# Performance work log

Hardware: AMD Instinct MI355X
Metric: run time of the kernel (lower is better)

Reference implementation:

```python
import jax, jax.numpy as jnp
import numpy as np
from jax import lax

B, T, FEAT = 8, 512, 128
D_MODEL, D_STATE, D_INNER, DT_RANK = 128, 16, 256, 8
N_LAYERS, NUM_CLASSES = 10, 35
FLAT = 64 * (FEAT // 4)  # 2048


def setup_inputs():
    keys = iter(jax.random.split(jax.random.key(0), 48))
    def nrm(shape, s=0.05):
        return jax.random.normal(next(keys), shape, jnp.float32) * s
    inp = {}
    inp['x'] = jax.random.normal(next(keys), (B, T, FEAT), jnp.float32)
    inp['lengths'] = jax.random.randint(next(keys), (B,), 0, T)
    inp['conv_w1'] = nrm((32, 1, 3, 3)); inp['conv_b1'] = nrm((32,))
    inp['bn1_s'] = 1.0 + nrm((32,)); inp['bn1_b'] = nrm((32,))
    inp['conv_w2'] = nrm((32, 32, 3, 3)); inp['conv_b2'] = nrm((32,))
    inp['bn2_s'] = 1.0 + nrm((32,)); inp['bn2_b'] = nrm((32,))
    inp['conv_w3'] = nrm((64, 32, 3, 3)); inp['conv_b3'] = nrm((64,))
    inp['bn3_s'] = 1.0 + nrm((64,)); inp['bn3_b'] = nrm((64,))
    inp['conv_w4'] = nrm((64, 64, 3, 3)); inp['conv_b4'] = nrm((64,))
    inp['bn4_s'] = 1.0 + nrm((64,)); inp['bn4_b'] = nrm((64,))
    inp['proj_w'] = nrm((D_MODEL, FLAT), 0.02); inp['proj_b'] = nrm((D_MODEL,))
    inp['proj_ln_s'] = jnp.ones((D_MODEL,)); inp['proj_ln_b'] = jnp.zeros((D_MODEL,))
    L = N_LAYERS
    inp['blk_ln_s'] = jnp.ones((L, D_MODEL)); inp['blk_ln_b'] = jnp.zeros((L, D_MODEL))
    inp['in_w'] = nrm((L, 2 * D_INNER, D_MODEL))
    inp['cw'] = nrm((L, D_INNER, 4)); inp['cb'] = nrm((L, D_INNER))
    inp['xp_w'] = nrm((L, DT_RANK + 2 * D_STATE, D_INNER))
    inp['dt_w'] = nrm((L, D_INNER, DT_RANK))
    inp['dt_b'] = nrm((L, D_INNER)) - 4.0  # softplus(-4) ~ 0.018: realistic small dt
    inp['A_log'] = jnp.tile(jnp.log(jnp.arange(1, D_STATE + 1, dtype=jnp.float32))[None, None, :], (L, D_INNER, 1))
    inp['Dp'] = jnp.ones((L, D_INNER))
    inp['out_w'] = nrm((L, D_MODEL, D_INNER))
    inp['pre_ln_s'] = jnp.ones((D_MODEL,)); inp['pre_ln_b'] = jnp.zeros((D_MODEL,))
    inp['cls_w1'] = nrm((D_MODEL // 2, D_MODEL)); inp['cls_b1'] = nrm((D_MODEL // 2,))
    inp['cls_w2'] = nrm((NUM_CLASSES, D_MODEL // 2)); inp['cls_b2'] = nrm((NUM_CLASSES,))
    return inp


def _ln(x, s, b):
    m = jnp.mean(x, -1, keepdims=True)
    v = jnp.mean((x - m) ** 2, -1, keepdims=True)
    return (x - m) * lax.rsqrt(v + 1e-5) * s + b


def _conv2d(x, w, b):
    y = lax.conv_general_dilated(x, w, (1, 1), 'SAME', dimension_numbers=('NCHW', 'OIHW', 'NCHW'))
    return y + b[None, :, None, None]


def _bn(x, s, b):  # eval-mode BatchNorm folded to per-channel affine
    return x * s[None, :, None, None] + b[None, :, None, None]


def _pool(x, kh, kw):
    return lax.reduce_window(x, -jnp.inf, lax.max, (1, 1, kh, kw), (1, 1, kh, kw), 'VALID')


def _mamba(x, in_w, cw, cb, xp_w, dt_w, dt_b, A_log, Dp, out_w):
    bb = x.shape[0]
    xz = jnp.einsum('btd,ed->bte', x, in_w)                  # [B,T,2*d_inner]
    xm, z = jnp.split(xz, 2, axis=-1)
    # causal depthwise conv1d (torch pads both sides by 3 then truncates to T == left-pad 3)
    xc = lax.conv_general_dilated(xm.transpose(0, 2, 1), cw[:, None, :], (1,), [(3, 0)],
                                  dimension_numbers=('NCH', 'OIH', 'NCH'), feature_group_count=D_INNER)
    xc = jax.nn.silu(xc + cb[None, :, None]).transpose(0, 2, 1)  # [B,T,d_inner]
    dbc = jnp.einsum('btd,ed->bte', xc, xp_w)
    dt, Bm, Cm = jnp.split(dbc, [DT_RANK, DT_RANK + D_STATE], axis=-1)
    dt = jax.nn.softplus(jnp.einsum('btr,dr->btd', dt, dt_w) + dt_b)  # [B,T,d_inner]
    A = -jnp.exp(A_log)                                      # [d_inner,d_state]
    dA = jnp.exp(dt[..., None] * A)                          # [B,T,d,n]
    dBu = (dt * xc)[..., None] * Bm[:, :, None, :]           # [B,T,d,n]
    def step(h, inp):
        dA_t, dBu_t, C_t = inp
        h = dA_t * h + dBu_t
        return h, jnp.einsum('bdn,bn->bd', h, C_t)
    h0 = jnp.zeros((bb, D_INNER, D_STATE), x.dtype)
    _, ys = lax.scan(step, h0, (dA.transpose(1, 0, 2, 3), dBu.transpose(1, 0, 2, 3), Cm.transpose(1, 0, 2)))
    y = ys.transpose(1, 0, 2) + Dp * xc
    y = y * jax.nn.silu(z)
    return jnp.einsum('btd,ed->bte', y, out_w)


def _forward(x, lengths, conv_w1, conv_b1, bn1_s, bn1_b, conv_w2, conv_b2, bn2_s, bn2_b,
             conv_w3, conv_b3, bn3_s, bn3_b, conv_w4, conv_b4, bn4_s, bn4_b,
             proj_w, proj_b, proj_ln_s, proj_ln_b, blk_ln_s, blk_ln_b,
             in_w, cw, cb, xp_w, dt_w, dt_b, A_log, Dp, out_w,
             pre_ln_s, pre_ln_b, cls_w1, cls_b1, cls_w2, cls_b2):
    h = x.transpose(0, 2, 1)[:, None]                        # [B,1,F,T]
    h = jax.nn.silu(_bn(_conv2d(h, conv_w1, conv_b1), bn1_s, bn1_b))
    h = jax.nn.silu(_bn(_conv2d(h, conv_w2, conv_b2), bn2_s, bn2_b))
    h = _pool(h, 2, 2)
    h = jax.nn.silu(_bn(_conv2d(h, conv_w3, conv_b3), bn3_s, bn3_b))
    h = jax.nn.silu(_bn(_conv2d(h, conv_w4, conv_b4), bn4_s, bn4_b))
    h = _pool(h, 2, 1)                                       # [B,64,F/4,T/2]
    h = h.transpose(0, 3, 1, 2).reshape(h.shape[0], h.shape[3], -1)  # [B,T',64*F/4]
    h = jax.nn.silu(_ln(jnp.einsum('btf,df->btd', h, proj_w) + proj_b, proj_ln_s, proj_ln_b))
    for i in range(N_LAYERS):
        h = h + _mamba(_ln(h, blk_ln_s[i], blk_ln_b[i]), in_w[i], cw[i], cb[i], xp_w[i],
                       dt_w[i], dt_b[i], A_log[i], Dp[i], out_w[i])
    h = _ln(h, pre_ln_s, pre_ln_b)
    t_lens = jnp.clip(lengths // 2, 1)
    mask = (jnp.arange(h.shape[1])[None, :] < t_lens[:, None]).astype(h.dtype)[..., None]
    pooled = (h * mask).sum(1) / jnp.clip(mask.sum(1), 1.0)
    c = jax.nn.silu(jnp.einsum('bd,hd->bh', pooled, cls_w1) + cls_b1)
    return jnp.einsum('bh,ch->bc', c, cls_w2) + cls_b2


def reference(x, lengths, conv_w1, conv_b1, bn1_s, bn1_b, conv_w2, conv_b2, bn2_s, bn2_b,
              conv_w3, conv_b3, bn3_s, bn3_b, conv_w4, conv_b4, bn4_s, bn4_b,
              proj_w, proj_b, proj_ln_s, proj_ln_b, blk_ln_s, blk_ln_b,
              in_w, cw, cb, xp_w, dt_w, dt_b, A_log, Dp, out_w,
              pre_ln_s, pre_ln_b, cls_w1, cls_b1, cls_w2, cls_b2):
    return _forward(x, lengths, conv_w1, conv_b1, bn1_s, bn1_b, conv_w2, conv_b2, bn2_s, bn2_b,
                    conv_w3, conv_b3, bn3_s, bn3_b, conv_w4, conv_b4, bn4_s, bn4_b,
                    proj_w, proj_b, proj_ln_s, proj_ln_b, blk_ln_s, blk_ln_b,
                    in_w, cw, cb, xp_w, dt_w, dt_b, A_log, Dp, out_w,
                    pre_ln_s, pre_ln_b, cls_w1, cls_b1, cls_w2, cls_b2)
```

## Files before the change

### kernel.cpp

```cpp
#include <hip/hip_runtime.h>
#include <math.h>

#define B_ 8
#define T_ 512
#define FEAT_ 128
#define TP 256
#define DM 128
#define DI 256
#define DS 16
#define DTR 8
#define NL 10

typedef _Float16 h2 __attribute__((ext_vector_type(2)));
typedef unsigned int uint32;

__device__ __forceinline__ float fsilu(float x){ return x / (1.f + __expf(-x)); }
__device__ __forceinline__ float fsoftplus(float x){ return (x > 20.f) ? x : log1pf(__expf(x)); }

__device__ __forceinline__ uint32 pack_h2(float a, float b){
  union { h2 h; uint32 u; } cv;
  cv.h[0] = (_Float16)a; cv.h[1] = (_Float16)b;
  return cv.u;
}
__device__ __forceinline__ h2 as_h2(uint32 u){
  union { uint32 u; h2 h; } cv; cv.u = u; return cv.h;
}

template<int CTRL>
__device__ __forceinline__ float dpp_ror(float x){
  int v = __builtin_amdgcn_update_dpp(0, __float_as_int(x), CTRL, 0xF, 0xF, false);
  return __int_as_float(v);
}
__device__ __forceinline__ float rsum16(float x){
  x += dpp_ror<0x121>(x);
  x += dpp_ror<0x122>(x);
  x += dpp_ror<0x124>(x);
  x += dpp_ror<0x128>(x);
  return x;
}

__global__ void k_transpose_x(const float* __restrict__ x, float* __restrict__ xT){
  int idx = blockIdx.x*256 + threadIdx.x;
  if(idx >= B_*FEAT_*T_) return;
  int t = idx % T_; int f = (idx/T_) % FEAT_; int b = idx/(T_*FEAT_);
  xT[idx] = x[((size_t)b*T_ + t)*FEAT_ + f];
}

__device__ __forceinline__ void wt_one(const float* __restrict__ w, float* __restrict__ o,
                                       int idx, int CO, int CIN){
  int k = idx % 9; int ci = (idx/9) % CIN; int co = idx/(9*CIN);
  o[((size_t)(ci*(CO>>3) + (co>>3)))*72 + (co&7)*9 + k] = w[idx];
}
__device__ __forceinline__ void wt_pack(const float* __restrict__ w, uint32* __restrict__ o,
                                        int idx, int CO, int CIN){
  int CIN2 = CIN >> 1;
  int k = idx % 9; int ci2 = (idx/9) % CIN2; int co = idx/(9*CIN2);
  float f0 = w[((size_t)co*CIN + 2*ci2 + 0)*9 + k];
  float f1 = w[((size_t)co*CIN + 2*ci2 + 1)*9 + k];
  o[((size_t)(ci2*(CO>>3) + (co>>3)))*72 + (co&7)*9 + k] = pack_h2(f0, f1);
}
__global__ void k_wt_all(const float* __restrict__ w1, const float* __restrict__ w2,
                         const float* __restrict__ w3, const float* __restrict__ w4,
                         float* __restrict__ o1, uint32* __restrict__ o2,
                         uint32* __restrict__ o3, uint32* __restrict__ o4){
  int idx = blockIdx.x*256 + threadIdx.x;
  if(idx < 288){ wt_one(w1, o1, idx, 32, 1); return; }
  idx -= 288;
  if(idx < 4608){ wt_pack(w2, o2, idx, 32, 32); return; }
  idx -= 4608;
  if(idx < 9216){ wt_pack(w3, o3, idx, 64, 32); return; }
  idx -= 9216;
  if(idx < 18432){ wt_pack(w4, o4, idx, 64, 64); return; }
}

template<int CIN, int CO, int CPW, int CIG, int COG>
__global__ __launch_bounds__(256) void k_conv_t4(const float* __restrict__ in,
     const float* __restrict__ wt, const float* __restrict__ cb,
     const float* __restrict__ bs, const float* __restrict__ bb,
     float* __restrict__ out, int H, int W){
  constexpr int NS = CO/CPW;
  __shared__ __align__(16) float tile[CIG*360];
  int tid = threadIdx.x;
  int lane = tid & 63;
  int wav = __builtin_amdgcn_readfirstlane(tid >> 6);
  int wpr = W >> 4, hpr = H >> 4;
  int idx = blockIdx.x;
  int cog = idx % COG; idx /= COG;
  int tj = idx % wpr; idx /= wpr;
  int ti = idx % hpr; int b = idx / hpr;
  int i0 = ti*16, j0 = tj*16;
  int r = lane & 15, cg = lane >> 4;
  int wslot = cog*4 + wav;
  const float* wbase = wt + (size_t)wslot*72;
  float acc[CPW][4] = {};
  for(int cig = 0; cig < CIN; cig += CIG){
    __syncthreads();
    for(int u = tid; u < CIG*324; u += 256){
      int ci = u / 324; int rem = u - ci*324; int rr = rem / 18; int cc = rem - rr*18;
      int gi = i0 - 1 + rr, gj = j0 - 1 + cc;
      float v = 0.f;
      if(gi >= 0 && gi < H && gj >= 0 && gj < W)
        v = in[((size_t)(b*CIN + cig + ci)*H + gi)*W + gj];
      tile[ci*360 + rr*20 + cc] = v;
    }
    __syncthreads();
    for(int ci = 0; ci < CIG; ci++){
      const float4* wp4 = (const float4*)(wbase + (size_t)(cig+ci)*(NS*72));
      float4 w4q[18];
      #pragma unroll
      for(int q=0;q<18;q++) w4q[q] = wp4[q];
      const float* wf = (const float*)w4q;
      #pragma unroll
      for(int kh=0;kh<3;kh++){
        float4 a = *(const float4*)&tile[ci*360 + (r+kh)*20 + cg*4];
        float4 bv = *(const float4*)&tile[ci*360 + (r+kh)*20 + cg*4 + 4];
        float v[6] = {a.x,a.y,a.z,a.w,bv.x,bv.y};
        #pragma unroll
        for(int co=0;co<CPW;co++){
          #pragma unroll
          for(int kw=0;kw<3;kw++){
            float wv = wf[co*9 + kh*3 + kw];
            #pragma unroll
            for(int u2=0;u2<4;u2++)
              acc[co][u2] = fmaf(wv, v[kw+u2], acc[co][u2]);
          }
        }
      }
    }
  }
  int i = i0 + r;
  #pragma unroll
  for(int co=0; co<CPW; co++){
    int c = cog*(4*CPW) + wav*CPW + co;
    float s = bs[c], bias = cb[c]*s + bb[c];
    float4 o;
    o.x = fsilu(acc[co][0]*s + bias);
    o.y = fsilu(acc[co][1]*s + bias);
    o.z = fsilu(acc[co][2]*s + bias);
    o.w = fsilu(acc[co][3]*s + bias);
    *(float4*)&out[((size_t)(b*CO + c)*H + i)*W + j0 + cg*4] = o;
  }
}

template<int CIN2, int CO, int CPW, int CIG2, int COG>
__global__ __launch_bounds__(256) void k_conv_t7(const float* __restrict__ in,
     const uint32* __restrict__ wt, const float* __restrict__ cb,
     const float* __restrict__ bs, const float* __restrict__ bb,
     float* __restrict__ out, int H, int W){
  constexpr int NS = CO/CPW;
  __shared__ __align__(16) uint32 tile[CIG2*360];
  int tid = threadIdx.x;
  int lane = tid & 63;
  int wav = __builtin_amdgcn_readfirstlane(tid >> 6);
  int wpr = W >> 4, hpr = H >> 4;
  int idx = blockIdx.x;
  int cog = idx % COG; idx /= COG;
  int tj = idx % wpr; idx /= wpr;
  int ti = idx % hpr; int b = idx / hpr;
  int i0 = ti*16, j0 = tj*16;
  int r = lane & 15, cg = lane >> 4;
  int wslot = cog*4 + wav;
  const uint32* wbase = wt + (size_t)wslot*72;
  float acc[CPW][4] = {};
  for(int c2g = 0; c2g < CIN2; c2g += CIG2){
    __syncthreads();
    for(int u = tid; u < CIG2*324; u += 256){
      int ci2 = u / 324; int rem = u - ci2*324; int rr = rem / 18; int cc = rem - rr*18;
      int gi = i0 - 1 + rr, gj = j0 - 1 + cc;
      float v0 = 0.f, v1 = 0.f;
      if(gi >= 0 && gi < H && gj >= 0 && gj < W){
        const float* p = in + ((size_t)(b*(CIN2*2) + (c2g+ci2)*2)*H + gi)*W + gj;
        v0 = p[0];
        v1 = p[(size_t)H*W];
      }
      tile[ci2*360 + rr*20 + cc] = pack_h2(v0, v1);
    }
    __syncthreads();
    for(int ci2 = 0; ci2 < CIG2; ci2++){
      const uint4* wp4 = (const uint4*)(wbase + (size_t)(c2g+ci2)*(NS*72));
      uint4 w4q[18];
      #pragma unroll
      for(int q=0;q<18;q++) w4q[q] = wp4[q];
      const uint32* wf = (const uint32*)w4q;
      h2 v[3][6];
      #pragma unroll
      for(int kh=0;kh<3;kh++){
        const uint32* trow = &tile[ci2*360 + (r+kh)*20 + cg*4];
        uint4 a4 = *(const uint4*)trow;
        v[kh][0]=as_h2(a4.x); v[kh][1]=as_h2(a4.y);
        v[kh][2]=as_h2(a4.z); v[kh][3]=as_h2(a4.w);
        v[kh][4]=as_h2(trow[4]); v[kh][5]=as_h2(trow[5]);
      }
      #pragma unroll
      for(int co=0;co<CPW;co++){
        #pragma unroll
        for(int kh=0;kh<3;kh++){
          #pragma unroll
          for(int kw=0;kw<3;kw++){
            h2 wv = as_h2(wf[co*9 + kh*3 + kw]);
            #pragma unroll
            for(int u2=0;u2<4;u2++)
              acc[co][u2] = __builtin_amdgcn_fdot2(wv, v[kh][kw+u2], acc[co][u2], false);
          }
        }
      }
    }
  }
  int i = i0 + r;
  #pragma unroll
  for(int co=0; co<CPW; co++){
    int c = cog*(4*CPW) + wav*CPW + co;
    float s = bs[c], bias = cb[c]*s + bb[c];
    float4 o;
    o.x = fsilu(acc[co][0]*s + bias);
    o.y = fsilu(acc[co][1]*s + bias);
    o.z = fsilu(acc[co][2]*s + bias);
    o.w = fsilu(acc[co][3]*s + bias);
    *(float4*)&out[((size_t)(b*CO + c)*H + i)*W + j0 + cg*4] = o;
  }
}

__global__ void k_pool2x2(const float* __restrict__ in, float* __restrict__ out,
                          int C, int Hi, int Wi){
  int Ho = Hi>>1, Wo = Wi>>1;
  int total = B_*C*Ho*Wo;
  int idx = blockIdx.x*256 + threadIdx.x;
  if(idx >= total) return;
  int j = idx % Wo; int i = (idx/Wo)%Ho; int c = (idx/(Wo*Ho))%C; int b = idx/(Wo*Ho*C);
  const float* p = in + (((size_t)(b*C+c)*Hi + 2*i)*Wi + 2*j);
  out[idx] = fmaxf(fmaxf(p[0], p[1]), fmaxf(p[Wi], p[Wi+1]));
}

__global__ __launch_bounds__(256) void k_proj(const float* __restrict__ R0,
    const float* __restrict__ W, float* __restrict__ pbuf){
  __shared__ __align__(16) float As[16][33];
  __shared__ __align__(16) float Ws[16][68];
  int tid = threadIdx.x;
  int n0 = blockIdx.x*64, m0 = blockIdx.y*32;
  int kc = blockIdx.z;
  int b = m0 >> 8;
  int t_base = m0 & 255;
  int tx = tid&15, ty = tid>>4;
  float acc[2][4] = {};
  for(int k0=0; k0<256; k0+=16){
    int kg0 = kc*256 + k0;
    if(tid < 128){
      int row = tid>>2, cq = (tid&3)*4;
      #pragma unroll
      for(int c2=0;c2<4;c2++){
        int k = kg0 + cq + c2;
        int c = k>>5, hh = k&31;
        const float* p = R0 + (((size_t)(b*64+c)*64 + 2*hh)*256 + t_base + row);
        As[cq+c2][row] = fmaxf(p[0], p[256]);
      }
    } else {
      int u = tid - 128; int n = u>>1, cq = (u&1)*8;
      const float* wp = W + (size_t)(n0+n)*2048 + kg0 + cq;
      float4 v0 = *(const float4*)wp, v1 = *(const float4*)(wp+4);
      Ws[cq+0][n]=v0.x; Ws[cq+1][n]=v0.y; Ws[cq+2][n]=v0.z; Ws[cq+3][n]=v0.w;
      Ws[cq+4][n]=v1.x; Ws[cq+5][n]=v1.y; Ws[cq+6][n]=v1.z; Ws[cq+7][n]=v1.w;
    }
    __syncthreads();
    #pragma unroll
    for(int kk=0;kk<16;kk++){
      float a0 = As[kk][ty*2+0];
      float a1 = As[kk][ty*2+1];
      float4 w4 = *(const float4*)&Ws[kk][tx*4];
      float wv4[4] = {w4.x,w4.y,w4.z,w4.w};
      #pragma unroll
      for(int j=0;j<4;j++){
        acc[0][j] = fmaf(a0, wv4[j], acc[0][j]);
        acc[1][j] = fmaf(a1, wv4[j], acc[1][j]);
      }
    }
    __syncthreads();
  }
  float* pb = pbuf + (size_t)kc*2048*DM;
  #pragma unroll
  for(int iu=0;iu<2;iu++){
    int m = m0 + ty*2 + iu;
    #pragma unroll
    for(int j=0;j<4;j++){
      int n = n0 + tx*4 + j;
      pb[(size_t)m*DM + n] = acc[iu][j];
    }
  }
}

__global__ void k_lnp(const float* __restrict__ pbuf, const float* __restrict__ bias,
                      const float* __restrict__ g, const float* __restrict__ b,
                      float* __restrict__ out){
  int row = blockIdx.x;
  int t = threadIdx.x;
  float v0 = bias[t], v1 = bias[t+64];
  #pragma unroll
  for(int kc=0;kc<8;kc++){
    const float* p = pbuf + ((size_t)kc*2048 + row)*DM;
    v0 += p[t]; v1 += p[t+64];
  }
  float s = v0 + v1;
  #pragma unroll
  for(int m=32;m>=1;m>>=1) s += __shfl_xor(s, m);
  float mean = s * (1.f/128.f);
  float e0 = v0-mean, e1 = v1-mean;
  float q = e0*e0 + e1*e1;
  #pragma unroll
  for(int m=32;m>=1;m>>=1) q += __shfl_xor(q, m);
  float inv = rsqrtf(q*(1.f/128.f) + 1e-5f);
  float o0 = fsilu(e0*inv*g[t] + b[t]);
  float o1 = fsilu(e1*inv*g[t+64] + b[t+64]);
  float* po = out + (size_t)row*DM;
  po[t] = o0; po[t+64] = o1;
}

template<int SILU>
__global__ void k_ln(const float* __restrict__ in, const float* __restrict__ g,
                     const float* __restrict__ b, float* __restrict__ out){
  int row = blockIdx.x;
  int t = threadIdx.x;
  const float* p = in + (size_t)row*DM;
  float v0 = p[t], v1 = p[t+64];
  float s = v0 + v1;
  #pragma unroll
  for(int m=32;m>=1;m>>=1) s += __shfl_xor(s, m);
  float mean = s * (1.f/128.f);
  float e0 = v0-mean, e1 = v1-mean;
  float q = e0*e0 + e1*e1;
  #pragma unroll
  for(int m=32;m>=1;m>>=1) q += __shfl_xor(q, m);
  float inv = rsqrtf(q*(1.f/128.f) + 1e-5f);
  float o0 = e0*inv*g[t] + b[t];
  float o1 = e1*inv*g[t+64] + b[t+64];
  if(SILU){ o0 = fsilu(o0); o1 = fsilu(o1); }
  float* po = out + (size_t)row*DM;
  po[t] = o0; po[t+64] = o1;
}

__global__ __launch_bounds__(256) void k_lnxz(const float* __restrict__ hbuf,
    const float* __restrict__ g, const float* __restrict__ bb,
    const float* __restrict__ W, float* __restrict__ out){
  __shared__ __align__(16) float lns[32][132];
  __shared__ __align__(16) float Ws[16][68];
  int tid = threadIdx.x;
  int n0 = blockIdx.x*64, m0 = blockIdx.y*32;
  for(int u=tid; u<1024; u+=256){
    int row = u>>5, c4 = (u&31)*4;
    float4 v = *(const float4*)(hbuf + (size_t)(m0+row)*DM + c4);
    lns[row][c4] = v.x; lns[row][c4+1] = v.y; lns[row][c4+2] = v.z; lns[row][c4+3] = v.w;
  }
  __syncthreads();
  {
    int lane = tid & 63, wv = tid >> 6;
    for(int rr = wv; rr < 32; rr += 4){
      float v0 = lns[rr][lane], v1 = lns[rr][lane+64];
      float s = v0+v1;
      #pragma unroll
      for(int mm=32;mm>=1;mm>>=1) s += __shfl_xor(s,mm);
      float mean = s*(1.f/128.f);
      float e0 = v0-mean, e1 = v1-mean;
      float q = e0*e0+e1*e1;
      #pragma unroll
      for(int mm=32;mm>=1;mm>>=1) q += __shfl_xor(q,mm);
      float inv = rsqrtf(q*(1.f/128.f)+1e-5f);
      lns[rr][lane]    = e0*inv*g[lane] + bb[lane];
      lns[rr][lane+64] = e1*inv*g[lane+64] + bb[lane+64];
    }
  }
  __syncthreads();
  int tx = tid&15, ty = tid>>4;
  float acc[2][4] = {};
  for(int k0=0;k0<128;k0+=16){
    {
      int n = tid>>2, c4 = (tid&3)*4;
      float4 v = *(const float4*)(W + (size_t)(n0+n)*DM + k0 + c4);
      Ws[c4+0][n]=v.x; Ws[c4+1][n]=v.y; Ws[c4+2][n]=v.z; Ws[c4+3][n]=v.w;
    }
    __syncthreads();
    #pragma unroll
    for(int kk=0;kk<16;kk++){
      float a0 = lns[ty*2+0][k0+kk];
      float a1 = lns[ty*2+1][k0+kk];
      float4 w4 = *(const float4*)&Ws[kk][tx*4];
      float wv4[4] = {w4.x,w4.y,w4.z,w4.w};
      #pragma unroll
      for(int j=0;j<4;j++){
        acc[0][j] = fmaf(a0, wv4[j], acc[0][j]);
        acc[1][j] = fmaf(a1, wv4[j], acc[1][j]);
      }
    }
    __syncthreads();
  }
  #pragma unroll
  for(int iu=0;iu<2;iu++){
    int m = m0 + ty*2 + iu;
    float* po = out + (size_t)m*512 + n0 + tx*4;
    #pragma unroll
    for(int j=0;j<4;j++) po[j] = acc[iu][j];
  }
}

__global__ __launch_bounds__(256) void k_xproj8(const float* __restrict__ xz,
    const float* __restrict__ cw, const float* __restrict__ cb,
    const float* __restrict__ xpw, const float* __restrict__ dtw,
    const float* __restrict__ dtb_, float* __restrict__ xc_g,
    float* __restrict__ dbc_g, float* __restrict__ dt_g){
  __shared__ float xzs[11][64];
  __shared__ float As[64][9];
  __shared__ float Wp[64][41];
  __shared__ float dtin[8][9];
  __shared__ float dtw_s[256][9];
  int tid = threadIdx.x;
  int row0 = blockIdx.x*8; int b = row0 >> 8; int t0 = row0 & 255;
  int rA = tid & 7, cgA = tid >> 3;
  int dlC = tid & 63, rqC = tid >> 6;
  float acc0 = 0.f, acc1 = 0.f;
  for(int ch=0; ch<4; ch++){
    int d0 = ch*64;
    __syncthreads();
    for(int u=tid; u<11*64; u+=256){
      int rr = u>>6, dl = u&63;
      int t = t0 + rr - 3;
      xzs[rr][dl] = (t >= 0) ? xz[((size_t)(b*TP)+t)*512 + d0 + dl] : 0.f;
    }
    for(int u=tid; u<40*64; u+=256){
      int nn = u>>6, dk = u&63;
      Wp[dk][nn] = xpw[(size_t)nn*DI + d0 + dk];
    }
    __syncthreads();
    {
      float cw0 = cw[(d0+dlC)*4+0], cw1 = cw[(d0+dlC)*4+1];
      float cw2 = cw[(d0+dlC)*4+2], cw3 = cw[(d0+dlC)*4+3];
      float cbv = cb[d0+dlC];
      #pragma unroll
      for(int i=0;i<2;i++){
        int rr = rqC*2 + i;
        float a = cbv;
        a = fmaf(cw0, xzs[rr+0][dlC], a);
        a = fmaf(cw1, xzs[rr+1][dlC], a);
        a = fmaf(cw2, xzs[rr+2][dlC], a);
        a = fmaf(cw3, xzs[rr+3][dlC], a);
        float v = fsilu(a);
        As[dlC][rr] = v;
        xc_g[((size_t)row0 + rr)*DI + d0 + dlC] = v;
      }
    }
    __syncthreads();
    for(int dk=0; dk<64; dk++){
      float a = As[dk][rA];
      acc0 = fmaf(a, Wp[dk][cgA], acc0);
      if(cgA < 8) acc1 = fmaf(a, Wp[dk][cgA+32], acc1);
    }
  }
  if(cgA < 8){
    dtin[rA][cgA] = acc0;
    dbc_g[((size_t)row0 + rA)*40 + cgA + 32] = acc1;
  } else {
    dbc_g[((size_t)row0 + rA)*40 + cgA] = acc0;
  }
  for(int u=tid; u<256*8; u+=256) dtw_s[u>>3][u&7] = dtw[u];
  __syncthreads();
  {
    int d = tid;
    float bias = dtb_[d];
    float w8[8];
    #pragma unroll
    for(int k=0;k<8;k++) w8[k] = dtw_s[d][k];
    #pragma unroll
    for(int r2=0;r2<8;r2++){
      float a = bias;
      #pragma unroll
      for(int k=0;k<8;k++) a = fmaf(dtin[r2][k], w8[k], a);
      dt_g[((size_t)row0 + r2)*DI + d] = fsoftplus(a);
    }
  }
}

__global__ __launch_bounds__(1024) void k_scan4(const float* __restrict__ dtb,
      const float* __restrict__ xc, const float* __restrict__ xz,
      const float* __restrict__ dbc, const float* __restrict__ A_log,
      const float* __restrict__ Dp, float* __restrict__ y){
  __shared__ float dt_s[TP][8], xc_s[TP][8];
  __shared__ float Bs[TP][16], Cs[TP][16];
  __shared__ float Eb[8][128], Pb[8][128];
  int tid = threadIdx.x;
  int c = tid >> 7, gl = (tid >> 4) & 7, n = tid & 15;
  int dblk = blockIdx.x & 31, b = blockIdx.x >> 5;
  int d0 = dblk*8;
  size_t rbase = (size_t)b*TP;
  for(int u=tid; u<TP*8; u+=1024){
    int tt = u>>3, gg = u&7;
    size_t r = rbase + tt;
    dt_s[tt][gg] = dtb[r*DI + d0 + gg];
    xc_s[tt][gg] = xc [r*DI + d0 + gg];
  }
  for(int u=tid; u<TP*16; u+=1024){
    int tt = u>>4, nn = u&15;
    size_t r = rbase + tt;
    Bs[tt][nn] = dbc[r*40 + 8  + nn];
    Cs[tt][nn] = dbc[r*40 + 24 + nn];
  }
  __syncthreads();
  int d = d0 + gl;
  float An = -__expf(A_log[d*DS + n]);
  float h = 0.f, dtsum = 0.f;
  int tA = c*32;
  float hc[32], ev[32];
  #pragma unroll
  for(int i=0;i<32;i++){
    int t = tA + i;
    float dtv = dt_s[t][gl];
    dtsum += dtv;
    float e = __expf(dtv*An);
    ev[i] = e;
    h = fmaf(e, h, dtv*xc_s[t][gl]*Bs[t][n]);
    hc[i] = h*Cs[t][n];
  }
  Eb[c][gl*16+n] = h;
  Pb[c][gl*16+n] = __expf(An*dtsum);
  __syncthreads();
  float g = 0.f;
  for(int cp=0; cp<c; cp++)
    g = fmaf(Pb[cp][gl*16+n], g, Eb[cp][gl*16+n]);
  float Dpd = Dp[d];
  #pragma unroll
  for(int i=0;i<32;i++){
    int t = tA + i;
    g *= ev[i];
    float p = rsum16(hc[i] + g*Cs[t][n]);
    if(n==0){
      float zv = xz[(rbase+t)*512 + DI + d];
      float xcv = xc_s[t][gl];
      y[(rbase+t)*DI + d] = (p + Dpd*xcv) * fsilu(zv);
    }
  }
}

__global__ __launch_bounds__(256) void k_out16(const float* __restrict__ A,
    const float* __restrict__ W, float* __restrict__ C){
  __shared__ float As[16][17];
  __shared__ __align__(16) float Ws[16][68];
  int tid = threadIdx.x;
  int n0 = blockIdx.x*64, m0 = blockIdx.y*16;
  int tx = tid&15, ty = tid>>4;
  float acc[4] = {};
  for(int k0=0;k0<256;k0+=16){
    {
      int row = tid>>4, kk = tid&15;
      As[kk][row] = A[(size_t)(m0+row)*DI + k0 + kk];
    }
    {
      int n = tid>>2, cq = (tid&3)*4;
      float4 v = *(const float4*)(W + (size_t)(n0+n)*DI + k0 + cq);
      Ws[cq+0][n]=v.x; Ws[cq+1][n]=v.y; Ws[cq+2][n]=v.z; Ws[cq+3][n]=v.w;
    }
    __syncthreads();
    #pragma unroll
    for(int kk=0;kk<16;kk++){
      float a0 = As[kk][ty];
      float4 w4 = *(const float4*)&Ws[kk][tx*4];
      acc[0] = fmaf(a0, w4.x, acc[0]);
      acc[1] = fmaf(a0, w4.y, acc[1]);
      acc[2] = fmaf(a0, w4.z, acc[2]);
      acc[3] = fmaf(a0, w4.w, acc[3]);
    }
    __syncthreads();
  }
  int m = m0 + ty;
  float* cp = &C[(size_t)m*DM + n0 + tx*4];
  cp[0] += acc[0]; cp[1] += acc[1]; cp[2] += acc[2]; cp[3] += acc[3];
}

__global__ void k_head(const float* __restrict__ hln, const int* __restrict__ lengths,
                       const float* __restrict__ w1, const float* __restrict__ b1,
                       const float* __restrict__ w2, const float* __restrict__ b2,
                       float* __restrict__ out){
  __shared__ float pooled[DM];
  __shared__ float cbuf[64];
  int b = blockIdx.x, tid = threadIdx.x;
  int tl = lengths[b] >> 1; if(tl < 1) tl = 1;
  float s = 0.f;
  const float* p = hln + (size_t)b*TP*DM + tid;
  for(int t=0;t<tl;t++) s += p[(size_t)t*DM];
  pooled[tid] = s / (float)tl;
  __syncthreads();
  if(tid < 64){
    float a = b1[tid];
    const float* wp = w1 + tid*DM;
    for(int k=0;k<DM;k++) a = fmaf(pooled[k], wp[k], a);
    cbuf[tid] = fsilu(a);
  }
  __syncthreads();
  if(tid < 35){
    float a = b2[tid];
    const float* wp = w2 + tid*64;
    for(int k=0;k<64;k++) a = fmaf(cbuf[k], wp[k], a);
    out[b*35+tid] = a;
  }
}

extern "C" void kernel_launch(void* const* d_in, const int* in_sizes, int n_in,
                              void* d_out, int out_size, void* d_ws, size_t ws_size,
                              hipStream_t stream){
  (void)in_sizes; (void)n_in; (void)out_size; (void)ws_size;
  const float* x        = (const float*)d_in[0];
  const int*   lengths  = (const int*)  d_in[1];
  const float* conv_w1  = (const float*)d_in[2];  const float* conv_b1 = (const float*)d_in[3];
  const float* bn1_s    = (const float*)d_in[4];  const float* bn1_b   = (const float*)d_in[5];
  const float* conv_w2  = (const float*)d_in[6];  const float* conv_b2 = (const float*)d_in[7];
  const float* bn2_s    = (const float*)d_in[8];  const float* bn2_b   = (const float*)d_in[9];
  const float* conv_w3  = (const float*)d_in[10]; const float* conv_b3 = (const float*)d_in[11];
  const float* bn3_s    = (const float*)d_in[12]; const float* bn3_b   = (const float*)d_in[13];
  const float* conv_w4  = (const float*)d_in[14]; const float* conv_b4 = (const float*)d_in[15];
  const float* bn4_s    = (const float*)d_in[16]; const float* bn4_b   = (const float*)d_in[17];
  const float* proj_w   = (const float*)d_in[18]; const float* proj_b  = (const float*)d_in[19];
  const float* proj_ln_s= (const float*)d_in[20]; const float* proj_ln_b=(const float*)d_in[21];
  const float* blk_ln_s = (const float*)d_in[22]; const float* blk_ln_b =(const float*)d_in[23];
  const float* in_w     = (const float*)d_in[24];
  const float* cw       = (const float*)d_in[25]; const float* cbv     = (const float*)d_in[26];
  const float* xp_w     = (const float*)d_in[27];
  const float* dt_w     = (const float*)d_in[28]; const float* dt_b    = (const float*)d_in[29];
  const float* A_log    = (const float*)d_in[30]; const float* Dp      = (const float*)d_in[31];
  const float* out_w    = (const float*)d_in[32];
  const float* pre_ln_s = (const float*)d_in[33]; const float* pre_ln_b= (const float*)d_in[34];
  const float* cls_w1   = (const float*)d_in[35]; const float* cls_b1  = (const float*)d_in[36];
  const float* cls_w2   = (const float*)d_in[37]; const float* cls_b2  = (const float*)d_in[38];

  float* ws   = (float*)d_ws;
  float* R0   = ws;
  float* R1   = R0 + 16777216;
  float* xT   = R1 + 16777216;
  float* hbuf = xT + 524288;
  float* lnb  = hbuf + 262144;
  float* xzb  = lnb + 262144;
  float* xcb  = xzb + 1048576;
  float* dbcb = xcb + 524288;
  float* dtbb = dbcb + 81920;
  float* yb   = dtbb + 524288;
  float* wt1  = yb + 524288;
  uint32* wt2h = (uint32*)(wt1 + 288);
  uint32* wt3h = wt2h + 4608;
  uint32* wt4h = wt3h + 9216;

  k_wt_all<<<128, 256, 0, stream>>>(conv_w1, conv_w2, conv_w3, conv_w4,
                                    wt1, wt2h, wt3h, wt4h);

  k_transpose_x<<<2048, 256, 0, stream>>>(x, xT);
  k_conv_t4<1,32,8,1,1><<<8*8*32, 256, 0, stream>>>(xT, wt1, conv_b1, bn1_s, bn1_b, R0, 128, 512);
  k_conv_t7<16,32,8,4,1><<<8*8*32, 256, 0, stream>>>(R0, wt2h, conv_b2, bn2_s, bn2_b, R1, 128, 512);
  k_pool2x2<<<(8*32*64*256)/256, 256, 0, stream>>>(R1, R0, 32, 128, 512);
  k_conv_t7<16,64,8,4,2><<<8*4*16*2, 256, 0, stream>>>(R0, wt3h, conv_b3, bn3_s, bn3_b, R1, 64, 256);
  k_conv_t7<32,64,8,4,2><<<8*4*16*2, 256, 0, stream>>>(R1, wt4h, conv_b4, bn4_s, bn4_b, R0, 64, 256);

  {
    dim3 gd(2, 64, 8);
    k_proj<<<gd, 256, 0, stream>>>(R0, proj_w, R1);
  }
  k_lnp<<<2048, 64, 0, stream>>>(R1, proj_b, proj_ln_s, proj_ln_b, hbuf);

  for(int i=0;i<NL;i++){
    { dim3 gd(8, 64);
      k_lnxz<<<gd, 256, 0, stream>>>(hbuf, blk_ln_s + i*DM, blk_ln_b + i*DM,
                                     in_w + (size_t)i*512*DM, xzb); }
    k_xproj8<<<256, 256, 0, stream>>>(xzb, cw + (size_t)i*DI*4, cbv + i*DI,
                                      xp_w + (size_t)i*40*DI, dt_w + (size_t)i*DI*DTR,
                                      dt_b + i*DI, xcb, dbcb, dtbb);
    k_scan4<<<256, 1024, 0, stream>>>(dtbb, xcb, xzb, dbcb, A_log + (size_t)i*DI*DS, Dp + i*DI, yb);
    { dim3 gd(2, 128);
      k_out16<<<gd, 256, 0, stream>>>(yb, out_w + (size_t)i*DM*DI, hbuf); }
  }

  k_ln<0><<<2048, 64, 0, stream>>>(hbuf, pre_ln_s, pre_ln_b, lnb);
  k_head<<<8, 128, 0, stream>>>(lnb, lengths, cls_w1, cls_b1, cls_w2, cls_b2, (float*)d_out);
}
```

Baseline: 1.154 ms.

## Prefetch conv input slabs into registers, fuse final LayerNorm into head, widen CIG2

The t7 conv kernel now loads the next input-channel slab into registers while computing on the current shared-memory slab, a software pipeline intended to hide global load latency. The channel-group size per slab doubles from 4 to 8, so there are fewer barriers at the cost of more shared memory and registers. The separate final LayerNorm kernel is folded into the head kernel, which normalizes and pools only the valid timesteps, removing one launch and a full pass over the activations. The conv3 weight packing is rewritten oddly (wrong CO in k_wt_all, then corrected by an extra k_wt3 launch), which adds one small kernel launch.

```diff
diff --git a/kernel.cpp b/kernel.cpp
--- a/kernel.cpp
+++ b/kernel.cpp
@@ -68,9 +68,13 @@
   idx -= 288;
   if(idx < 4608){ wt_pack(w2, o2, idx, 32, 32); return; }
   idx -= 4608;
-  if(idx < 9216){ wt_pack(w3, o3, idx, 64, 32); return; }
+  if(idx < 9216){ wt_pack(w3, o3, idx, 32, 32); return; }
   idx -= 9216;
   if(idx < 18432){ wt_pack(w4, o4, idx, 64, 64); return; }
+}
+__global__ void k_wt3(const float* __restrict__ w3, uint32* __restrict__ o3){
+  int idx = blockIdx.x*256 + threadIdx.x;
+  if(idx < 9216) wt_pack(w3, o3, idx, 64, 32);
 }
 
 template<int CIN, int CO, int CPW, int CIG, int COG>
@@ -148,6 +152,9 @@
      const float* __restrict__ bs, const float* __restrict__ bb,
      float* __restrict__ out, int H, int W){
   constexpr int NS = CO/CPW;
+  constexpr int NSLAB = CIN2/CIG2;
+  constexpr int NEL = CIG2*324;
+  constexpr int NLD = (NEL + 255)/256;
   __shared__ __align__(16) uint32 tile[CIG2*360];
   int tid = threadIdx.x;
   int lane = tid & 63;
@@ -162,22 +169,46 @@
   int wslot = cog*4 + wav;
   const uint32* wbase = wt + (size_t)wslot*72;
   float acc[CPW][4] = {};
-  for(int c2g = 0; c2g < CIN2; c2g += CIG2){
-    __syncthreads();
-    for(int u = tid; u < CIG2*324; u += 256){
-      int ci2 = u / 324; int rem = u - ci2*324; int rr = rem / 18; int cc = rem - rr*18;
-      int gi = i0 - 1 + rr, gj = j0 - 1 + cc;
+  float r0[NLD], r1[NLD];
+
+  auto LOAD = [&](int c2g){
+    #pragma unroll
+    for(int l=0;l<NLD;l++){
+      int u = tid + l*256;
       float v0 = 0.f, v1 = 0.f;
-      if(gi >= 0 && gi < H && gj >= 0 && gj < W){
-        const float* p = in + ((size_t)(b*(CIN2*2) + (c2g+ci2)*2)*H + gi)*W + gj;
-        v0 = p[0];
-        v1 = p[(size_t)H*W];
-      }
-      tile[ci2*360 + rr*20 + cc] = pack_h2(v0, v1);
-    }
-    __syncthreads();
-    for(int ci2 = 0; ci2 < CIG2; ci2++){
-      const uint4* wp4 = (const uint4*)(wbase + (size_t)(c2g+ci2)*(NS*72));
+      if(u < NEL){
+        int ci2 = u/324; int rem = u - ci2*324; int rr = rem/18; int cc = rem - rr*18;
+        int gi = i0 - 1 + rr, gj = j0 - 1 + cc;
+        if(gi >= 0 && gi < H && gj >= 0 && gj < W){
+          const float* p = in + ((size_t)(b*(CIN2*2) + (c2g+ci2)*2)*H + gi)*W + gj;
+          v0 = p[0];
+          v1 = p[(size_t)H*W];
+        }
+      }
+      r0[l] = v0; r1[l] = v1;
+    }
+  };
+  auto WRITE = [&](){
+    #pragma unroll
+    for(int l=0;l<NLD;l++){
+      int u = tid + l*256;
+      if(u < NEL){
+        int ci2 = u/324; int rem = u - ci2*324; int rr = rem/18; int cc = rem - rr*18;
+        tile[ci2*360 + rr*20 + cc] = pack_h2(r0[l], r1[l]);
+      }
+    }
+  };
+
+  LOAD(0);
+  for(int s=0; s<NSLAB; s++){
+    __syncthreads();
+    WRITE();
+    __syncthreads();
+    if(s+1 < NSLAB) LOAD((s+1)*CIG2);
+    #pragma unroll
+    for(int ci2=0; ci2<CIG2; ci2++){
+      int sci2 = s*CIG2 + ci2;
+      const uint4* wp4 = (const uint4*)(wbase + (size_t)sci2*(NS*72));
       uint4 w4q[18];
       #pragma unroll
       for(int q=0;q<18;q++) w4q[q] = wp4[q];
@@ -309,29 +340,6 @@
   float inv = rsqrtf(q*(1.f/128.f) + 1e-5f);
   float o0 = fsilu(e0*inv*g[t] + b[t]);
   float o1 = fsilu(e1*inv*g[t+64] + b[t+64]);
-  float* po = out + (size_t)row*DM;
-  po[t] = o0; po[t+64] = o1;
-}
-
-template<int SILU>
-__global__ void k_ln(const float* __restrict__ in, const float* __restrict__ g,
-                     const float* __restrict__ b, float* __restrict__ out){
-  int row = blockIdx.x;
-  int t = threadIdx.x;
-  const float* p = in + (size_t)row*DM;
-  float v0 = p[t], v1 = p[t+64];
-  float s = v0 + v1;
-  #pragma unroll
-  for(int m=32;m>=1;m>>=1) s += __shfl_xor(s, m);
-  float mean = s * (1.f/128.f);
-  float e0 = v0-mean, e1 = v1-mean;
-  float q = e0*e0 + e1*e1;
-  #pragma unroll
-  for(int m=32;m>=1;m>>=1) q += __shfl_xor(q, m);
-  float inv = rsqrtf(q*(1.f/128.f) + 1e-5f);
-  float o0 = e0*inv*g[t] + b[t];
-  float o1 = e1*inv*g[t+64] + b[t+64];
-  if(SILU){ o0 = fsilu(o0); o1 = fsilu(o1); }
   float* po = out + (size_t)row*DM;
   po[t] = o0; po[t+64] = o1;
 }
@@ -570,18 +578,37 @@
   cp[0] += acc[0]; cp[1] += acc[1]; cp[2] += acc[2]; cp[3] += acc[3];
 }
 
-__global__ void k_head(const float* __restrict__ hln, const int* __restrict__ lengths,
-                       const float* __restrict__ w1, const float* __restrict__ b1,
-                       const float* __restrict__ w2, const float* __restrict__ b2,
-                       float* __restrict__ out){
+__global__ __launch_bounds__(256) void k_head2(const float* __restrict__ h,
+    const int* __restrict__ lengths, const float* __restrict__ g,
+    const float* __restrict__ bv, const float* __restrict__ w1,
+    const float* __restrict__ b1, const float* __restrict__ w2,
+    const float* __restrict__ b2, float* __restrict__ out){
+  __shared__ float pp[4][128];
   __shared__ float pooled[DM];
   __shared__ float cbuf[64];
   int b = blockIdx.x, tid = threadIdx.x;
+  int lane = tid & 63, wv = tid >> 6;
   int tl = lengths[b] >> 1; if(tl < 1) tl = 1;
-  float s = 0.f;
-  const float* p = hln + (size_t)b*TP*DM + tid;
-  for(int t=0;t<tl;t++) s += p[(size_t)t*DM];
-  pooled[tid] = s / (float)tl;
+  float p0 = 0.f, p1 = 0.f;
+  for(int t = wv; t < tl; t += 4){
+    const float* row = h + ((size_t)(b*TP)+t)*DM;
+    float v0 = row[lane], v1 = row[lane+64];
+    float s = v0+v1;
+    #pragma unroll
+    for(int mm=32;mm>=1;mm>>=1) s += __shfl_xor(s,mm);
+    float mean = s*(1.f/128.f);
+    float e0 = v0-mean, e1 = v1-mean;
+    float q = e0*e0+e1*e1;
+    #pragma unroll
+    for(int mm=32;mm>=1;mm>>=1) q += __shfl_xor(q,mm);
+    float inv = rsqrtf(q*(1.f/128.f)+1e-5f);
+    p0 += e0*inv*g[lane] + bv[lane];
+    p1 += e1*inv*g[lane+64] + bv[lane+64];
+  }
+  pp[wv][lane] = p0; pp[wv][lane+64] = p1;
+  __syncthreads();
+  if(tid < 128)
+    pooled[tid] = (pp[0][tid]+pp[1][tid]+pp[2][tid]+pp[3][tid]) / (float)tl;
   __syncthreads();
   if(tid < 64){
     float a = b1[tid];
@@ -643,13 +670,14 @@
 
   k_wt_all<<<128, 256, 0, stream>>>(conv_w1, conv_w2, conv_w3, conv_w4,
                                     wt1, wt2h, wt3h, wt4h);
+  k_wt3<<<36, 256, 0, stream>>>(conv_w3, wt3h);
 
   k_transpose_x<<<2048, 256, 0, stream>>>(x, xT);
   k_conv_t4<1,32,8,1,1><<<8*8*32, 256, 0, stream>>>(xT, wt1, conv_b1, bn1_s, bn1_b, R0, 128, 512);
-  k_conv_t7<16,32,8,4,1><<<8*8*32, 256, 0, stream>>>(R0, wt2h, conv_b2, bn2_s, bn2_b, R1, 128, 512);
+  k_conv_t7<16,32,8,8,1><<<8*8*32, 256, 0, stream>>>(R0, wt2h, conv_b2, bn2_s, bn2_b, R1, 128, 512);
   k_pool2x2<<<(8*32*64*256)/256, 256, 0, stream>>>(R1, R0, 32, 128, 512);
-  k_conv_t7<16,64,8,4,2><<<8*4*16*2, 256, 0, stream>>>(R0, wt3h, conv_b3, bn3_s, bn3_b, R1, 64, 256);
-  k_conv_t7<32,64,8,4,2><<<8*4*16*2, 256, 0, stream>>>(R1, wt4h, conv_b4, bn4_s, bn4_b, R0, 64, 256);
+  k_conv_t7<16,64,8,8,2><<<8*4*16*2, 256, 0, stream>>>(R0, wt3h, conv_b3, bn3_s, bn3_b, R1, 64, 256);
+  k_conv_t7<32,64,8,8,2><<<8*4*16*2, 256, 0, stream>>>(R1, wt4h, conv_b4, bn4_s, bn4_b, R0, 64, 256);
 
   {
     dim3 gd(2, 64, 8);
@@ -669,6 +697,6 @@
       k_out16<<<gd, 256, 0, stream>>>(yb, out_w + (size_t)i*DM*DI, hbuf); }
   }
 
-  k_ln<0><<<2048, 64, 0, stream>>>(hbuf, pre_ln_s, pre_ln_b, lnb);
-  k_head<<<8, 128, 0, stream>>>(lnb, lengths, cls_w1, cls_b1, cls_w2, cls_b2, (float*)d_out);
-}
+  k_head2<<<8, 256, 0, stream>>>(hbuf, lengths, pre_ln_s, pre_ln_b,
+                                 cls_w1, cls_b1, cls_w2, cls_b2, (float*)d_out);
+}
```

New measurement: 1.128 ms. 2.3% less time.
